# Performance work log

Hardware: AMD Instinct MI355X
Metric: run time of the kernel (lower is better)

The kernel has to match this reference:

```python
import jax, jax.numpy as jnp
import numpy as np

# Module hyperparameters (init_kwargs)
TOP_K = 0.15          # fraction of pixels kept per row when step_percent=1
IGNORE_INDEX = 255

B, K, N, H, W = 8, 3, 8, 384, 384


def setup_inputs() -> dict:
    key = jax.random.key(0)
    k1, k2 = jax.random.split(key)
    # log-probabilities over K classes (nll_loss expects log-probs)
    logits = jax.random.normal(k1, (B, K, N, H, W), dtype=jnp.float32)
    inp = jax.nn.log_softmax(logits, axis=1)
    target = jax.random.randint(k2, (B, N, H, W), 0, K, dtype=jnp.int32)
    return {"input": inp, "target": target, "step_percent": 1}


def reference(input, target, step_percent):
    b, k, n, h, w = input.shape
    P = h * w
    x = input.reshape(b * n, k, P)           # (BN, K, P)
    t = target.reshape(b * n, P)             # (BN, P)

    # per-pixel NLL with ignore_index (ignored pixels contribute 0)
    mask = t != IGNORE_INDEX
    t_safe = jnp.where(mask, t, 0)
    nll = -jnp.take_along_axis(x, t_safe[:, None, :], axis=1)[:, 0, :]  # (BN, P)
    nll = jnp.where(mask, nll, jnp.zeros((), nll.dtype))

    # static k: step_percent is a Python scalar in the original forward
    sp = min(float(step_percent), 1.0)
    n_top_k = int(sp * TOP_K * P + (1.0 - sp) * P)

    top_k_loss, _ = jax.lax.top_k(nll, n_top_k)  # (BN, n_top_k)
    return jnp.mean(top_k_loss)
```

## Files before the change

### kernel.cpp

```cpp
#include <hip/hip_runtime.h>

#define BN    64
#define KCLS  3
#define PPIX  147456
#define NB1   4096

#define BPR    32
#define F4PB   (PPIX / 4 / BPR)

#define RS_THREADS 1024
#define RS_F4      (PPIX / 4 / RS_THREADS)
#define CAPS       8192

static const size_t OFF_NLL  = 0;
static const size_t OFF_GH   = (size_t)BN * PPIX * 4;
static const size_t OFF_ACC  = OFF_GH + (size_t)BN * NB1 * 4;
static const size_t OFF_DONE = OFF_ACC + 8;
static const size_t ZERO_END = OFF_DONE + 8;

__device__ __forceinline__ unsigned topk_count(const int* sp_ptr) {
    double sp = (double)sp_ptr[0];
    if (sp > 1.0) sp = 1.0;
    return (unsigned)(sp * 0.15 * (double)PPIX + (1.0 - sp) * (double)PPIX);
}

__device__ __forceinline__ float sel_nll(int t, float a, float b, float c) {
    float lp = (t == 0) ? a : ((t == 1) ? b : ((t == 2) ? c : 0.0f));
    return fmaxf(-lp, 0.0f);
}

__global__ __launch_bounds__(256) void k_hist1(
    const float* __restrict__ in, const int* __restrict__ tgt,
    float* __restrict__ nll, unsigned* __restrict__ cnt1)
{
    __shared__ unsigned lc[NB1];
    const int tid = threadIdx.x;
    for (int i = tid; i < NB1; i += 256) lc[i] = 0u;
    __syncthreads();

    const int row   = blockIdx.x / BPR;
    const int chunk = blockIdx.x % BPR;
    const float4* p0 = (const float4*)(in + (size_t)row * KCLS * PPIX);
    const float4* p1 = p0 + PPIX / 4;
    const float4* p2 = p1 + PPIX / 4;
    const int4*   t4 = (const int4*)(tgt + (size_t)row * PPIX);
    float4*       n4 = (float4*)(nll + (size_t)row * PPIX);
    const int base = chunk * F4PB;
    const bool tail = (tid < (F4PB - 4 * 256));

    int idx_c = base + tid;
    int4   t_c = t4[idx_c];
    float4 a_c = p0[idx_c];
    float4 b_c = p1[idx_c];
    float4 c_c = p2[idx_c];

    #pragma unroll
    for (int j = 0; j < 4; ++j) {
        int idx_n = 0;
        int4 t_n; float4 a_n, b_n, c_n;
        const bool have_next = (j < 3) || tail;
        if (have_next) {
            idx_n = base + (j + 1) * 256 + tid;
            t_n = t4[idx_n];
            a_n = p0[idx_n];
            b_n = p1[idx_n];
            c_n = p2[idx_n];
        }

        float4 v;
        v.x = sel_nll(t_c.x, a_c.x, b_c.x, c_c.x);
        v.y = sel_nll(t_c.y, a_c.y, b_c.y, c_c.y);
        v.z = sel_nll(t_c.z, a_c.z, b_c.z, c_c.z);
        v.w = sel_nll(t_c.w, a_c.w, b_c.w, c_c.w);
        n4[idx_c] = v;
        atomicAdd(&lc[__float_as_uint(v.x) >> 19], 1u);
        atomicAdd(&lc[__float_as_uint(v.y) >> 19], 1u);
        atomicAdd(&lc[__float_as_uint(v.z) >> 19], 1u);
        atomicAdd(&lc[__float_as_uint(v.w) >> 19], 1u);

        idx_c = idx_n; t_c = t_n; a_c = a_n; b_c = b_n; c_c = c_n;
    }

    if (tail) {
        float4 v;
        v.x = sel_nll(t_c.x, a_c.x, b_c.x, c_c.x);
        v.y = sel_nll(t_c.y, a_c.y, b_c.y, c_c.y);
        v.z = sel_nll(t_c.z, a_c.z, b_c.z, c_c.z);
        v.w = sel_nll(t_c.w, a_c.w, b_c.w, c_c.w);
        n4[idx_c] = v;
        atomicAdd(&lc[__float_as_uint(v.x) >> 19], 1u);
        atomicAdd(&lc[__float_as_uint(v.y) >> 19], 1u);
        atomicAdd(&lc[__float_as_uint(v.z) >> 19], 1u);
        atomicAdd(&lc[__float_as_uint(v.w) >> 19], 1u);
    }
    __syncthreads();

    unsigned* gc = cnt1 + (size_t)row * NB1;
    for (int i = tid; i < NB1; i += 256) {
        const unsigned cc = lc[i];
        if (cc) atomicAdd(&gc[i], cc);
    }
}

__global__ __launch_bounds__(RS_THREADS, 1) void k_rowselect(
    const float* __restrict__ nll, const unsigned* __restrict__ ghist,
    const int* __restrict__ sp, double* __restrict__ accum,
    unsigned* __restrict__ done, float* __restrict__ out)
{
    __shared__ float    stage[CAPS];
    __shared__ double   dd[RS_THREADS];
    __shared__ unsigned cs[RS_THREADS];
    __shared__ unsigned lc2[1024];
    __shared__ float    ls2[1024];
    __shared__ int s_b1, s_r1, s_lcnt, s_b2, s_r2;
    __shared__ double s_S0, s_S2;

    const int row = blockIdx.x;
    const int tid = threadIdx.x;

    const unsigned* ghr = ghist + (size_t)row * NB1;
    unsigned cl[4]; unsigned cacc = 0u;
    #pragma unroll
    for (int i = 0; i < 4; ++i) {
        cl[i] = ghr[NB1 - 1 - (tid * 4 + i)];
        cacc += cl[i];
    }
    cs[tid] = cacc;
    __syncthreads();
    for (int off = 1; off < RS_THREADS; off <<= 1) {
        unsigned t2 = (tid >= off) ? cs[tid - off] : 0u;
        __syncthreads();
        cs[tid] += t2;
        __syncthreads();
    }
    const unsigned k = topk_count(sp);
    {
        unsigned cum = tid ? cs[tid - 1] : 0u;
        #pragma unroll
        for (int i = 0; i < 4; ++i) {
            const unsigned cb = cl[i];
            if (cum < k && cum + cb >= k) {
                s_b1 = NB1 - 1 - (tid * 4 + i);
                s_r1 = (int)(k - cum);
            }
            cum += cb;
        }
    }
    if (tid == 0) s_lcnt = 0;
    __syncthreads();

    const unsigned b1 = (unsigned)s_b1;
    const unsigned lo = b1 << 19;
    const unsigned hi = (b1 + 1u) << 19;
    const float4* n4 = (const float4*)(nll + (size_t)row * PPIX);

    double acc = 0.0;
    #pragma unroll
    for (int j = 0; j < RS_F4; ++j) {
        const float4 f = n4[j * RS_THREADS + tid];
        const float vv[4] = {f.x, f.y, f.z, f.w};
        #pragma unroll
        for (int q = 0; q < 4; ++q) {
            const unsigned u = __float_as_uint(vv[q]);
            if (u >= hi) {
                acc += (double)vv[q];
            } else if (u >= lo) {
                const int s = atomicAdd(&s_lcnt, 1);
                if (s < CAPS) stage[s] = vv[q];
            }
        }
    }
    dd[tid] = acc;
    __syncthreads();
    for (int s = RS_THREADS / 2; s > 0; s >>= 1) {
        if (tid < s) dd[tid] += dd[tid + s];
        __syncthreads();
    }
    if (tid == 0) s_S0 = dd[0];
    int n = s_lcnt; if (n > CAPS) n = CAPS;

    lc2[tid] = 0u; ls2[tid] = 0.0f;
    __syncthreads();
    for (int i = tid; i < n; i += RS_THREADS) {
        const float v = stage[i];
        const unsigned key = (__float_as_uint(v) >> 9) & 0x3FFu;
        atomicAdd(&lc2[key], 1u);
        atomicAdd(&ls2[key], v);
    }
    __syncthreads();

    {
        const unsigned c2 = lc2[1023 - tid];
        const float    f2 = ls2[1023 - tid];
        cs[tid] = c2; dd[tid] = (double)f2;
        __syncthreads();
        for (int off = 1; off < RS_THREADS; off <<= 1) {
            unsigned tc = 0u; double td = 0.0;
            if (tid >= off) { tc = cs[tid - off]; td = dd[tid - off]; }
            __syncthreads();
            cs[tid] += tc; dd[tid] += td;
            __syncthreads();
        }
        const unsigned k2 = (unsigned)s_r1;
        const unsigned cum = tid ? cs[tid - 1] : 0u;
        const double   sS  = tid ? dd[tid - 1] : 0.0;
        if (cum < k2 && cum + c2 >= k2) {
            s_b2 = 1023 - tid;
            s_r2 = (int)(k2 - cum);
            s_S2 = sS;
        }
    }
    __syncthreads();

    const unsigned b2 = (unsigned)s_b2;
    if (tid < 512) { lc2[tid] = 0u; ls2[tid] = 0.0f; }
    __syncthreads();
    for (int i = tid; i < n; i += RS_THREADS) {
        const float v = stage[i];
        const unsigned bits = __float_as_uint(v);
        if (((bits >> 9) & 0x3FFu) == b2) {
            atomicAdd(&lc2[bits & 0x1FFu], 1u);
            atomicAdd(&ls2[bits & 0x1FFu], v);
        }
    }
    __syncthreads();
    {
        const unsigned c3 = (tid < 512) ? lc2[511 - tid] : 0u;
        const float    f3 = (tid < 512) ? ls2[511 - tid] : 0.0f;
        cs[tid] = c3; dd[tid] = (double)f3;
        __syncthreads();
        for (int off = 1; off < RS_THREADS; off <<= 1) {
            unsigned tc = 0u; double td = 0.0;
            if (tid >= off) { tc = cs[tid - off]; td = dd[tid - off]; }
            __syncthreads();
            cs[tid] += tc; dd[tid] += td;
            __syncthreads();
        }
        const unsigned k3 = (unsigned)s_r2;
        const unsigned cum = tid ? cs[tid - 1] : 0u;
        const double   S3  = tid ? dd[tid - 1] : 0.0;
        if (cum < k3 && cum + c3 >= k3) {
            const int      bin3 = 511 - tid;
            const unsigned r3   = k3 - cum;
            const float tval = __uint_as_float((b1 << 19) | (b2 << 9) | (unsigned)bin3);
            const double total = s_S0 + s_S2 + S3 + (double)r3 * (double)tval;
            atomicAdd(accum, total);
            __threadfence();
            const unsigned ticket =
                __hip_atomic_fetch_add(done, 1u, __ATOMIC_ACQ_REL, __HIP_MEMORY_SCOPE_AGENT);
            if (ticket == BN - 1) {
                const double a2 =
                    __hip_atomic_load(accum, __ATOMIC_RELAXED, __HIP_MEMORY_SCOPE_AGENT);
                out[0] = (float)(a2 / ((double)BN * (double)topk_count(sp)));
            }
        }
    }
}

extern "C" void kernel_launch(void* const* d_in, const int* in_sizes, int n_in,
                              void* d_out, int out_size, void* d_ws, size_t ws_size,
                              hipStream_t stream)
{
    (void)in_sizes; (void)n_in; (void)out_size; (void)ws_size;
    const float* in  = (const float*)d_in[0];
    const int*   tgt = (const int*)d_in[1];
    const int*   sp  = (const int*)d_in[2];

    char* ws = (char*)d_ws;
    float*    nll   = (float*)(ws + OFF_NLL);
    unsigned* ghist = (unsigned*)(ws + OFF_GH);
    double*   accum = (double*)(ws + OFF_ACC);
    unsigned* done  = (unsigned*)(ws + OFF_DONE);

    hipMemsetAsync(ws + OFF_GH, 0, ZERO_END - OFF_GH, stream);

    k_hist1    <<<BN * BPR, 256,        0, stream>>>(in, tgt, nll, ghist);
    k_rowselect<<<BN,       RS_THREADS, 0, stream>>>(nll, ghist, sp, accum, done,
                                                     (float*)d_out);
}
```

Before: 241.9 us.

## Split row-select pass across many blocks with last-block-done refinement

The second kernel changes from one 1024-thread block per row (64 blocks) to 32 blocks of 256 threads per row. Each block scans its chunk of the NLL row, adds up values above the threshold bin, and appends boundary-bin candidates to a global per-row buffer using wave-aggregated atomics. The last block to arrive for a row then runs the two refinement histogram passes. The goal is to fill the GPU during the bandwidth-heavy rescan of the NLL buffer, at the price of global atomics, counters and a serialized tail per row.

After: 869.3 us. 259% more time.

```diff
diff --git a/kernel.cpp b/kernel.cpp
--- a/kernel.cpp
+++ b/kernel.cpp
@@ -4,17 +4,20 @@
 #define KCLS  3
 #define PPIX  147456
 #define NB1   4096
+#define CAP   8192
 
 #define BPR    32
 #define F4PB   (PPIX / 4 / BPR)
 
-#define RS_THREADS 1024
-#define RS_F4      (PPIX / 4 / RS_THREADS)
-#define CAPS       8192
+#define SCOPE __HIP_MEMORY_SCOPE_AGENT
 
 static const size_t OFF_NLL  = 0;
-static const size_t OFF_GH   = (size_t)BN * PPIX * 4;
-static const size_t OFF_ACC  = OFF_GH + (size_t)BN * NB1 * 4;
+static const size_t OFF_CAND = OFF_NLL + (size_t)BN * PPIX * 4;
+static const size_t OFF_GH   = OFF_CAND + (size_t)BN * CAP * 4;
+static const size_t OFF_CCNT = OFF_GH + (size_t)BN * NB1 * 4;
+static const size_t OFF_SS   = OFF_CCNT + 256;
+static const size_t OFF_ARR  = OFF_SS + 512;
+static const size_t OFF_ACC  = OFF_ARR + 256;
 static const size_t OFF_DONE = OFF_ACC + 8;
 static const size_t ZERO_END = OFF_DONE + 8;
 
@@ -27,6 +30,19 @@
 __device__ __forceinline__ float sel_nll(int t, float a, float b, float c) {
     float lp = (t == 0) ? a : ((t == 1) ? b : ((t == 2) ? c : 0.0f));
     return fmaxf(-lp, 0.0f);
+}
+
+__device__ __forceinline__ int ld_ai32(const int* p) {
+    return __hip_atomic_load(p, __ATOMIC_RELAXED, SCOPE);
+}
+__device__ __forceinline__ float ld_af32(const float* p) {
+    return __hip_atomic_load(p, __ATOMIC_RELAXED, SCOPE);
+}
+__device__ __forceinline__ double ld_af64(const double* p) {
+    return __hip_atomic_load(p, __ATOMIC_RELAXED, SCOPE);
+}
+__device__ __forceinline__ void st_af32(float* p, float v) {
+    __hip_atomic_store(p, v, __ATOMIC_RELAXED, SCOPE);
 }
 
 __global__ __launch_bounds__(256) void k_hist1(
@@ -102,62 +118,69 @@
     }
 }
 
-__global__ __launch_bounds__(RS_THREADS, 1) void k_rowselect(
+__global__ __launch_bounds__(256) void k_finish(
     const float* __restrict__ nll, const unsigned* __restrict__ ghist,
-    const int* __restrict__ sp, double* __restrict__ accum,
+    const int* __restrict__ sp, float* __restrict__ cand,
+    int* __restrict__ ccnt, double* __restrict__ st_S,
+    unsigned* __restrict__ arr, double* __restrict__ accum,
     unsigned* __restrict__ done, float* __restrict__ out)
 {
-    __shared__ float    stage[CAPS];
-    __shared__ double   dd[RS_THREADS];
-    __shared__ unsigned cs[RS_THREADS];
+    __shared__ unsigned cs[256];
+    __shared__ double   dd[256];
     __shared__ unsigned lc2[1024];
     __shared__ float    ls2[1024];
-    __shared__ int s_b1, s_r1, s_lcnt, s_b2, s_r2;
-    __shared__ double s_S0, s_S2;
-
-    const int row = blockIdx.x;
-    const int tid = threadIdx.x;
+    __shared__ int s_b1, s_r1, s_last, s_b2, s_r2;
+    __shared__ double s_S2;
+
+    const int tid   = threadIdx.x;
+    const int row   = blockIdx.x / BPR;
+    const int chunk = blockIdx.x % BPR;
 
     const unsigned* ghr = ghist + (size_t)row * NB1;
-    unsigned cl[4]; unsigned cacc = 0u;
-    #pragma unroll
-    for (int i = 0; i < 4; ++i) {
-        cl[i] = ghr[NB1 - 1 - (tid * 4 + i)];
-        cacc += cl[i];
-    }
-    cs[tid] = cacc;
-    __syncthreads();
-    for (int off = 1; off < RS_THREADS; off <<= 1) {
-        unsigned t2 = (tid >= off) ? cs[tid - off] : 0u;
+    {
+        unsigned cl[16]; unsigned cacc = 0u;
+        const int base = tid * 16;
+        #pragma unroll
+        for (int i = 0; i < 16; ++i) {
+            cl[i] = ghr[NB1 - 1 - (base + i)];
+            cacc += cl[i];
+        }
+        cs[tid] = cacc;
         __syncthreads();
-        cs[tid] += t2;
-        __syncthreads();
-    }
-    const unsigned k = topk_count(sp);
-    {
+        for (int off = 1; off < 256; off <<= 1) {
+            unsigned t2 = (tid >= off) ? cs[tid - off] : 0u;
+            __syncthreads();
+            cs[tid] += t2;
+            __syncthreads();
+        }
+        const unsigned k = topk_count(sp);
         unsigned cum = tid ? cs[tid - 1] : 0u;
         #pragma unroll
-        for (int i = 0; i < 4; ++i) {
+        for (int i = 0; i < 16; ++i) {
             const unsigned cb = cl[i];
             if (cum < k && cum + cb >= k) {
-                s_b1 = NB1 - 1 - (tid * 4 + i);
+                s_b1 = NB1 - 1 - (base + i);
                 s_r1 = (int)(k - cum);
             }
             cum += cb;
         }
     }
-    if (tid == 0) s_lcnt = 0;
     __syncthreads();
 
     const unsigned b1 = (unsigned)s_b1;
     const unsigned lo = b1 << 19;
     const unsigned hi = (b1 + 1u) << 19;
     const float4* n4 = (const float4*)(nll + (size_t)row * PPIX);
+    int*   ccr = &ccnt[row];
+    float* cr  = cand + (size_t)row * CAP;
+    const int gbase = chunk * F4PB;
+    const int lane  = tid & 63;
 
     double acc = 0.0;
     #pragma unroll
-    for (int j = 0; j < RS_F4; ++j) {
-        const float4 f = n4[j * RS_THREADS + tid];
+    for (int j = 0; j < 5; ++j) {
+        if (j == 4 && tid >= (F4PB - 4 * 256)) break;
+        const float4 f = n4[gbase + j * 256 + tid];
         const float vv[4] = {f.x, f.y, f.z, f.w};
         #pragma unroll
         for (int q = 0; q < 4; ++q) {
@@ -165,36 +188,60 @@
             if (u >= hi) {
                 acc += (double)vv[q];
             } else if (u >= lo) {
-                const int s = atomicAdd(&s_lcnt, 1);
-                if (s < CAPS) stage[s] = vv[q];
+                const unsigned long long m = __ballot(1);
+                const int lead = (int)(__ffsll((long long)m) - 1);
+                int wb = 0;
+                if (lane == lead) wb = atomicAdd(ccr, __popcll(m));
+                wb = __shfl(wb, lead, 64);
+                const int slot = wb + __popcll(m & ((1ull << lane) - 1ull));
+                if (slot < CAP) st_af32(&cr[slot], vv[q]);
             }
         }
     }
     dd[tid] = acc;
     __syncthreads();
-    for (int s = RS_THREADS / 2; s > 0; s >>= 1) {
+    for (int s = 128; s > 0; s >>= 1) {
         if (tid < s) dd[tid] += dd[tid + s];
         __syncthreads();
     }
-    if (tid == 0) s_S0 = dd[0];
-    int n = s_lcnt; if (n > CAPS) n = CAPS;
-
-    lc2[tid] = 0u; ls2[tid] = 0.0f;
-    __syncthreads();
-    for (int i = tid; i < n; i += RS_THREADS) {
-        const float v = stage[i];
+    if (tid == 0) atomicAdd(&st_S[row], dd[0]);
+    __syncthreads();
+
+    if (tid == 0) {
+        __threadfence();
+        const unsigned t = __hip_atomic_fetch_add(&arr[row], 1u,
+                                                  __ATOMIC_ACQ_REL, SCOPE);
+        s_last = (t == (unsigned)(BPR - 1));
+    }
+    __syncthreads();
+    if (!s_last) return;
+
+    int n = ld_ai32(ccr); if (n > CAP) n = CAP;
+
+    for (int i = tid; i < 1024; i += 256) { lc2[i] = 0u; ls2[i] = 0.0f; }
+    __syncthreads();
+    for (int i = tid; i < n; i += 256) {
+        const float v = ld_af32(&cr[i]);
         const unsigned key = (__float_as_uint(v) >> 9) & 0x3FFu;
         atomicAdd(&lc2[key], 1u);
         atomicAdd(&ls2[key], v);
     }
     __syncthreads();
-
     {
-        const unsigned c2 = lc2[1023 - tid];
-        const float    f2 = ls2[1023 - tid];
-        cs[tid] = c2; dd[tid] = (double)f2;
+        unsigned cl2[4]; float slv[4];
+        unsigned cacc = 0u; double sacc = 0.0;
+        const int base = tid * 4;
+        #pragma unroll
+        for (int i = 0; i < 4; ++i) {
+            const int bin = 1023 - (base + i);
+            cl2[i] = lc2[bin];
+            slv[i] = ls2[bin];
+            cacc += cl2[i];
+            sacc += (double)slv[i];
+        }
+        cs[tid] = cacc; dd[tid] = sacc;
         __syncthreads();
-        for (int off = 1; off < RS_THREADS; off <<= 1) {
+        for (int off = 1; off < 256; off <<= 1) {
             unsigned tc = 0u; double td = 0.0;
             if (tid >= off) { tc = cs[tid - off]; td = dd[tid - off]; }
             __syncthreads();
@@ -202,21 +249,27 @@
             __syncthreads();
         }
         const unsigned k2 = (unsigned)s_r1;
-        const unsigned cum = tid ? cs[tid - 1] : 0u;
-        const double   sS  = tid ? dd[tid - 1] : 0.0;
-        if (cum < k2 && cum + c2 >= k2) {
-            s_b2 = 1023 - tid;
-            s_r2 = (int)(k2 - cum);
-            s_S2 = sS;
+        unsigned cum = tid ? cs[tid - 1] : 0u;
+        double   sS  = tid ? dd[tid - 1] : 0.0;
+        #pragma unroll
+        for (int i = 0; i < 4; ++i) {
+            const unsigned cb = cl2[i];
+            if (cum < k2 && cum + cb >= k2) {
+                s_b2 = 1023 - (base + i);
+                s_r2 = (int)(k2 - cum);
+                s_S2 = sS;
+            }
+            cum += cb;
+            sS  += (double)slv[i];
         }
     }
     __syncthreads();
 
     const unsigned b2 = (unsigned)s_b2;
-    if (tid < 512) { lc2[tid] = 0u; ls2[tid] = 0.0f; }
-    __syncthreads();
-    for (int i = tid; i < n; i += RS_THREADS) {
-        const float v = stage[i];
+    for (int i = tid; i < 512; i += 256) { lc2[i] = 0u; ls2[i] = 0.0f; }
+    __syncthreads();
+    for (int i = tid; i < n; i += 256) {
+        const float v = ld_af32(&cr[i]);
         const unsigned bits = __float_as_uint(v);
         if (((bits >> 9) & 0x3FFu) == b2) {
             atomicAdd(&lc2[bits & 0x1FFu], 1u);
@@ -225,11 +278,20 @@
     }
     __syncthreads();
     {
-        const unsigned c3 = (tid < 512) ? lc2[511 - tid] : 0u;
-        const float    f3 = (tid < 512) ? ls2[511 - tid] : 0.0f;
-        cs[tid] = c3; dd[tid] = (double)f3;
+        unsigned cl3[2]; float slv[2];
+        unsigned cacc = 0u; double sacc = 0.0;
+        const int base = tid * 2;
+        #pragma unroll
+        for (int i = 0; i < 2; ++i) {
+            const int bin = 511 - (base + i);
+            cl3[i] = lc2[bin];
+            slv[i] = ls2[bin];
+            cacc += cl3[i];
+            sacc += (double)slv[i];
+        }
+        cs[tid] = cacc; dd[tid] = sacc;
         __syncthreads();
-        for (int off = 1; off < RS_THREADS; off <<= 1) {
+        for (int off = 1; off < 256; off <<= 1) {
             unsigned tc = 0u; double td = 0.0;
             if (tid >= off) { tc = cs[tid - off]; td = dd[tid - off]; }
             __syncthreads();
@@ -237,22 +299,28 @@
             __syncthreads();
         }
         const unsigned k3 = (unsigned)s_r2;
-        const unsigned cum = tid ? cs[tid - 1] : 0u;
-        const double   S3  = tid ? dd[tid - 1] : 0.0;
-        if (cum < k3 && cum + c3 >= k3) {
-            const int      bin3 = 511 - tid;
-            const unsigned r3   = k3 - cum;
-            const float tval = __uint_as_float((b1 << 19) | (b2 << 9) | (unsigned)bin3);
-            const double total = s_S0 + s_S2 + S3 + (double)r3 * (double)tval;
-            atomicAdd(accum, total);
-            __threadfence();
-            const unsigned ticket =
-                __hip_atomic_fetch_add(done, 1u, __ATOMIC_ACQ_REL, __HIP_MEMORY_SCOPE_AGENT);
-            if (ticket == BN - 1) {
-                const double a2 =
-                    __hip_atomic_load(accum, __ATOMIC_RELAXED, __HIP_MEMORY_SCOPE_AGENT);
-                out[0] = (float)(a2 / ((double)BN * (double)topk_count(sp)));
+        unsigned cum = tid ? cs[tid - 1] : 0u;
+        double   S3  = tid ? dd[tid - 1] : 0.0;
+        #pragma unroll
+        for (int i = 0; i < 2; ++i) {
+            const unsigned cb = cl3[i];
+            if (cum < k3 && cum + cb >= k3) {
+                const int      bin3 = 511 - (base + i);
+                const unsigned r3   = k3 - cum;
+                const float tval = __uint_as_float((b1 << 19) | (b2 << 9) | (unsigned)bin3);
+                const double total = ld_af64(&st_S[row]) + s_S2 + S3
+                                   + (double)r3 * (double)tval;
+                atomicAdd(accum, total);
+                __threadfence();
+                const unsigned ticket = __hip_atomic_fetch_add(
+                    done, 1u, __ATOMIC_ACQ_REL, SCOPE);
+                if (ticket == BN - 1) {
+                    const double a2 = ld_af64(accum);
+                    out[0] = (float)(a2 / ((double)BN * (double)topk_count(sp)));
+                }
             }
+            cum += cb;
+            S3  += (double)slv[i];
         }
     }
 }
@@ -268,13 +336,17 @@
 
     char* ws = (char*)d_ws;
     float*    nll   = (float*)(ws + OFF_NLL);
+    float*    cand  = (float*)(ws + OFF_CAND);
     unsigned* ghist = (unsigned*)(ws + OFF_GH);
+    int*      ccnt  = (int*)(ws + OFF_CCNT);
+    double*   st_S  = (double*)(ws + OFF_SS);
+    unsigned* arr   = (unsigned*)(ws + OFF_ARR);
     double*   accum = (double*)(ws + OFF_ACC);
     unsigned* done  = (unsigned*)(ws + OFF_DONE);
 
     hipMemsetAsync(ws + OFF_GH, 0, ZERO_END - OFF_GH, stream);
 
-    k_hist1    <<<BN * BPR, 256,        0, stream>>>(in, tgt, nll, ghist);
-    k_rowselect<<<BN,       RS_THREADS, 0, stream>>>(nll, ghist, sp, accum, done,
-                                                     (float*)d_out);
-}
+    k_hist1 <<<BN * BPR, 256, 0, stream>>>(in, tgt, nll, ghist);
+    k_finish<<<BN * BPR, 256, 0, stream>>>(nll, ghist, sp, cand, ccnt, st_S,
+                                           arr, accum, done, (float*)d_out);
+}
```
